# Optimization experiments

Measured on AMD Instinct MI355X. Metric: run time of the kernel, lower is better.

## Reference

```python
import jax, jax.numpy as jnp
import numpy as np

E = 1024   # embed_dim
H = 16     # num_heads
D = E // H # head_dim = 64
P = 32     # project_dim
BS = 32768


def setup_inputs() -> dict:
    key0 = jax.random.key(0)
    ks = jax.random.split(key0, 16)
    s = 0.02
    inp = {
        "query": jax.random.normal(ks[0], (BS, E), jnp.float32),
        "key": jax.random.normal(ks[1], (BS, E), jnp.float32),
        "value": jax.random.normal(ks[2], (BS, E), jnp.float32),
        "attn_bias": jax.random.normal(ks[3], (BS, H), jnp.float32),
        # q/k/v embedding linears: [E, H*D]
        "Wq": jax.random.normal(ks[4], (E, H * D), jnp.float32) * s,
        "bq": jnp.zeros((H * D,), jnp.float32),
        "Wk": jax.random.normal(ks[5], (E, H * D), jnp.float32) * s,
        "bk": jnp.zeros((H * D,), jnp.float32),
        "Wv": jax.random.normal(ks[6], (E, H * D), jnp.float32) * s,
        "bv": jnp.zeros((H * D,), jnp.float32),
        # key/value low-rank projection linears: [E, H*P]
        "We": jax.random.normal(ks[7], (E, H * P), jnp.float32) * s,
        "be": jnp.zeros((H * P,), jnp.float32),
        "Wf": jax.random.normal(ks[8], (E, H * P), jnp.float32) * s,
        "bf": jnp.zeros((H * P,), jnp.float32),
        # feature_expand: [H, H*P]
        "Wfe": jax.random.normal(ks[9], (H, H * P), jnp.float32) * s,
        "bfe": jnp.zeros((H * P,), jnp.float32),
        # out_linear: [H*D, E]
        "Wo": jax.random.normal(ks[10], (H * D, E), jnp.float32) * s,
        "bo": jnp.zeros((E,), jnp.float32),
    }
    return inp


def reference(query, key, value, attn_bias,
              Wq, bq, Wk, bk, Wv, bv,
              We, be, Wf, bf, Wfe, bfe, Wo, bo):
    bs = query.shape[0]
    scale = 1.0 / np.sqrt(D).astype(np.float32)

    q = (query @ Wq + bq).reshape(bs, H, D)   # [bs, H, D]
    k = (key @ Wk + bk).reshape(bs, H, D)     # [bs, H, D]
    v = (value @ Wv + bv).reshape(bs, H, D)   # [bs, H, D]
    e = (key @ We + be).reshape(bs, H, P)     # [bs, H, P]
    f = (value @ Wf + bf).reshape(bs, H, P)   # [bs, H, P]

    # With tgt_len=src_len=1: q @ (e @ k)^T == (q.k) * e  (outer-product collapse)
    qk = jnp.einsum('bhd,bhd->bh', q, k)                     # [bs, H]
    bias = (attn_bias @ Wfe + bfe).reshape(bs, H, P)          # [bs, H, P]
    attn = scale * qk[..., None] * e + bias                   # [bs, H, P]
    attn = jax.nn.softmax(attn, axis=-1)                      # dropout p=0 (eval)

    # attn @ (f @ v) == (attn.f) * v
    af = jnp.einsum('bhp,bhp->bh', attn, f)                   # [bs, H]
    out = (af[..., None] * v).reshape(bs, H * D) @ Wo + bo    # [bs, E]
    return out
```

## Files before the change

### kernel.cpp

```cpp
#include <hip/hip_runtime.h>
#include <hip/hip_bf16.h>
#include <stdint.h>

#define BS_N 32768
#define E_DIM 1024

typedef __bf16 bf16x8 __attribute__((ext_vector_type(8)));
typedef float f32x4 __attribute__((ext_vector_type(4)));

__device__ __forceinline__ float asf(uint32_t u){ union{uint32_t u;float f;}x; x.u=u; return x.f; }
__device__ __forceinline__ uint32_t asu(float f){ union{float f;uint32_t u;}x; x.f=f; return x.u; }
__device__ __forceinline__ float blo(uint32_t u){ return asf(u<<16); }
__device__ __forceinline__ float bhi(uint32_t u){ return asf(u & 0xffff0000u); }
__device__ __forceinline__ uint16_t f2b(float f){
  uint32_t u = asu(f);
  u = u + 0x7fffu + ((u>>16)&1u);
  return (uint16_t)(u>>16);
}
__device__ __forceinline__ uint32_t pack2(float lo, float hi){
  return (uint32_t)f2b(lo) | ((uint32_t)f2b(hi)<<16);
}

#define GLD16(g, l) __builtin_amdgcn_global_load_lds( \
    (__attribute__((address_space(1))) const void*)(g), \
    (__attribute__((address_space(3))) void*)(l), 16, 0, 0)

#define BAR() __builtin_amdgcn_s_barrier()
#define LGKM0() do{ asm volatile("s_waitcnt lgkmcnt(0)" ::: "memory"); __builtin_amdgcn_sched_barrier(0); }while(0)
#define VMC4() do{ asm volatile("s_waitcnt vmcnt(4)" ::: "memory"); __builtin_amdgcn_sched_barrier(0); }while(0)
#define VMC0() do{ asm volatile("s_waitcnt vmcnt(0)" ::: "memory"); __builtin_amdgcn_sched_barrier(0); }while(0)

__global__ __launch_bounds__(256) void cast_bf16(const float4* __restrict__ in,
                                                 uint2* __restrict__ out, int n4){
  int i = blockIdx.x*256 + threadIdx.x;
  int stride = gridDim.x*256;
  for (; i < n4; i += stride){
    float4 v = in[i];
    uint2 o; o.x = pack2(v.x, v.y); o.y = pack2(v.z, v.w);
    out[i] = o;
  }
}

__global__ __launch_bounds__(256) void transpose_cast(const float* __restrict__ W,
                                                      uint16_t* __restrict__ WT,
                                                      int R, int C){
  __shared__ float tile[32][33];
  int c0 = blockIdx.x*32, r0 = blockIdx.y*32;
  int tx = threadIdx.x, ty = threadIdx.y;
  #pragma unroll
  for (int i=0;i<32;i+=8) tile[ty+i][tx] = W[(size_t)(r0+ty+i)*C + c0+tx];
  __syncthreads();
  #pragma unroll
  for (int i=0;i<32;i+=8) WT[(size_t)(c0+ty+i)*R + r0+tx] = f2b(tile[tx][ty+i]);
}

__global__ __launch_bounds__(256) void prep_ab(const float* __restrict__ ab,
                                               uint16_t* __restrict__ abp){
  int i = blockIdx.x*256 + threadIdx.x;
  int b = i >> 5, j = i & 31;
  abp[i] = f2b(j < 16 ? ab[b*16 + j] : 0.f);
}

__global__ __launch_bounds__(256) void prep_wfe(const float* __restrict__ Wfe,
                                                uint16_t* __restrict__ WfeTp){
  int i = blockIdx.x*256 + threadIdx.x;
  int n = i >> 5, j = i & 31;
  float v = (j < 16) ? Wfe[j*512 + n] : 0.f;
  WfeTp[n*32 + j] = f2b(v);
}

__global__ __launch_bounds__(256) void cat2(const float* __restrict__ a, int na,
                                            const float* __restrict__ b, int nb,
                                            float* __restrict__ o){
  int i = blockIdx.x*256 + threadIdx.x;
  if (i < na) o[i] = a[i];
  else if (i < na + nb) o[i] = b[i - na];
}

template<int BF16OUT>
__global__ __launch_bounds__(512, 2) void gemm256(const uint16_t* __restrict__ A,
                                                  const uint16_t* __restrict__ BT,
                                                  const float* __restrict__ bias,
                                                  void* __restrict__ Cp,
                                                  int N, int K){
  __shared__ alignas(16) uint16_t As_[2][16384];
  __shared__ alignas(16) uint16_t Bs_[2][16384];

  const int tid  = threadIdx.x;
  const int lane = tid & 63;
  const int w    = tid >> 6;
  const int wm   = w >> 2;
  const int wn   = w & 3;
  const int r    = lane & 15;
  const int kc   = lane >> 4;

  int bid = (int)blockIdx.x;
  int nwg = (int)gridDim.x;
  int cpx = nwg >> 3;
  int swz = (bid & 7)*cpx + (bid >> 3);
  const int rowTile = swz & 127;
  const int colTile = swz >> 7;
  const int row0 = rowTile << 8;
  const int col0 = colTile << 8;

  f32x4 acc[8][4];
  #pragma unroll
  for (int i=0;i<8;i++)
    #pragma unroll
    for (int j=0;j<4;j++){ f32x4 z = {0.f,0.f,0.f,0.f}; acc[i][j] = z; }

  const int NT = K >> 6;
  const size_t K2 = (size_t)K * 2;

  const int sr  = tid >> 3;
  const int scS = ((tid & 7) << 4) ^ ((sr & 7) << 4);
  const char* gA = (const char*)(A  + (size_t)row0 * K) + (size_t)sr*K2 + scS;
  const char* gB = (const char*)(BT + (size_t)col0 * K) + (size_t)sr*K2 + scS;
  char* ldsA = (char*)&As_[0][0];
  char* ldsB = (char*)&Bs_[0][0];

  #define STAGE_A(b, hh, u) do{ \
    const char* s_ = gA + (size_t)(hh)*(K2<<7) + ((size_t)(u)<<7); \
    char* d_ = ldsA + ((b)<<15) + ((hh)<<14) + (tid<<4); \
    GLD16(s_, d_); GLD16(s_ + (K2<<6), d_ + 8192); }while(0)
  #define STAGE_B(b, hh, u) do{ \
    const char* s_ = gB + (size_t)(hh)*(K2<<7) + ((size_t)(u)<<7); \
    char* d_ = ldsB + ((b)<<15) + ((hh)<<14) + (tid<<4); \
    GLD16(s_, d_); GLD16(s_ + (K2<<6), d_ + 8192); }while(0)

  const int rdKey = (kc << 4) ^ ((r & 7) << 4);
  const char* aR = ldsA + ((wm*128 + r) * 128);
  const char* bR = ldsB + ((wn*64  + r) * 128);

  bf16x8 afr[4][2], bf0[2][2], bf1[2][2];

  #define READ_A(QM) do{ \
    _Pragma("unroll") for (int fm=0; fm<4; ++fm) \
    _Pragma("unroll") for (int ks=0; ks<2; ++ks) \
      afr[fm][ks] = *(const bf16x8*)(aB + (QM)*8192 + fm*2048 + (rdKey ^ (ks<<6))); }while(0)
  #define READ_B(DST, QN) do{ \
    _Pragma("unroll") for (int fn=0; fn<2; ++fn) \
    _Pragma("unroll") for (int ks=0; ks<2; ++ks) \
      DST[fn][ks] = *(const bf16x8*)(bB + (QN)*4096 + fn*2048 + (rdKey ^ (ks<<6))); }while(0)
  #define MFMA16(QM, QN, BF) do{ \
    __builtin_amdgcn_s_setprio(1); \
    _Pragma("unroll") for (int ks=0; ks<2; ++ks) \
    _Pragma("unroll") for (int fm=0; fm<4; ++fm) \
    _Pragma("unroll") for (int fn=0; fn<2; ++fn) \
      acc[(QM)*4+fm][(QN)*2+fn] = __builtin_amdgcn_mfma_f32_16x16x32_bf16( \
        afr[fm][ks], BF[fn][ks], acc[(QM)*4+fm][(QN)*2+fn], 0, 0, 0); \
    __builtin_amdgcn_s_setprio(0); }while(0)

  STAGE_B(0,0,0); STAGE_B(0,1,0); STAGE_A(0,0,0); STAGE_A(0,1,0);
  if (NT > 1){ STAGE_B(1,0,1); STAGE_B(1,1,1); VMC4(); }
  else       { VMC0(); }
  BAR();

  for (int t = 0; t < NT; ++t){
    const int buf = t & 1;
    const char* aB = aR + (buf << 15);
    const char* bB = bR + (buf << 15);
    READ_A(0); READ_B(bf0, 0);
    if (t+1 < NT) STAGE_A(buf^1, 0, t+1);
    BAR(); LGKM0();
    MFMA16(0,0,bf0);
    BAR();
    READ_B(bf1, 1);
    if (t+1 < NT) STAGE_A(buf^1, 1, t+1);
    BAR(); LGKM0();
    MFMA16(0,1,bf1);
    BAR();
    READ_A(1);
    if (t+2 < NT) STAGE_B(buf, 0, t+2);
    BAR(); LGKM0();
    MFMA16(1,0,bf0);
    BAR();
    if (t+2 < NT) STAGE_B(buf, 1, t+2);
    BAR(); LGKM0();
    MFMA16(1,1,bf1);
    if (t+2 < NT) { VMC4(); } else { VMC0(); }
    BAR();
  }

  const int crow = row0 + wm*128 + ((lane>>4)<<2);
  const int ccol = col0 + wn*64 + (lane & 15);
  #pragma unroll
  for (int i=0;i<8;i++){
    #pragma unroll
    for (int n=0;n<4;n++){
      int col = ccol + n*16;
      float bv = bias[col];
      #pragma unroll
      for (int j=0;j<4;j++){
        float val = acc[i][n][j] + bv;
        int row = crow + i*16 + j;
        if (BF16OUT) ((uint16_t*)Cp)[(size_t)row*N + col] = f2b(val);
        else         ((float*)Cp)   [(size_t)row*N + col] = val;
      }
    }
  }
  #undef STAGE_A
  #undef STAGE_B
  #undef READ_A
  #undef READ_B
  #undef MFMA16
}

template<int BF16OUT>
__global__ __launch_bounds__(256) void gemm_bt(const uint16_t* __restrict__ A,
                                               const uint16_t* __restrict__ BT,
                                               const float* __restrict__ bias,
                                               void* __restrict__ Cp,
                                               int N, int K){
  __shared__ alignas(16) uint16_t As[128*32];
  __shared__ alignas(16) uint16_t Bs[128*32];
  const int tid  = threadIdx.x;
  const int lane = tid & 63;
  const int w    = tid >> 6;
  const int wr   = w >> 1, wc = w & 1;

  int bid = (int)blockIdx.x;
  int nwg = (int)gridDim.x;
  int cpx = nwg >> 3;
  int swz = (bid & 7)*cpx + (bid >> 3);
  int rowTile = swz & 255;
  int colTile = swz >> 8;
  const size_t row0 = (size_t)rowTile << 7;
  const int col0 = colTile << 7;

  f32x4 acc[4][4];
  #pragma unroll
  for (int m=0;m<4;m++)
    #pragma unroll
    for (int n=0;n<4;n++){ f32x4 z = {0.f,0.f,0.f,0.f}; acc[m][n] = z; }

  const int c0 = tid, c1 = tid + 256;
  const int ar0 = c0 >> 2, ao0 = (c0 & 3) << 4;
  const int ar1 = c1 >> 2, ao1 = (c1 & 3) << 4;
  const size_t K2 = (size_t)K * 2;
  const char* Ab = (const char*)(A  + row0 * (size_t)K);
  const char* Bb = (const char*)(BT + (size_t)col0 * (size_t)K);
  const char* gA0 = Ab + (size_t)ar0*K2 + ao0;
  const char* gA1 = Ab + (size_t)ar1*K2 + ao1;
  const char* gB0 = Bb + (size_t)ar0*K2 + ao0;
  const char* gB1 = Bb + (size_t)ar1*K2 + ao1;
  char* lA0 = (char*)As + c0*16;
  char* lA1 = (char*)As + c1*16;
  char* lB0 = (char*)Bs + c0*16;
  char* lB1 = (char*)Bs + c1*16;

  const int r = lane & 15, kc = lane >> 4;
  const char* aRd = (const char*)As + ((wr<<6) + r)*64 + (kc<<4);
  const char* bRd = (const char*)Bs + ((wc<<6) + r)*64 + (kc<<4);

  for (int kt = 0; kt < K; kt += 32){
    GLD16(gA0 + kt*2, lA0);
    GLD16(gA1 + kt*2, lA1);
    GLD16(gB0 + kt*2, lB0);
    GLD16(gB1 + kt*2, lB1);
    __syncthreads();
    bf16x8 a[4], b[4];
    #pragma unroll
    for (int m=0;m<4;m++) a[m] = *(const bf16x8*)(aRd + m*1024);
    #pragma unroll
    for (int n=0;n<4;n++) b[n] = *(const bf16x8*)(bRd + n*1024);
    #pragma unroll
    for (int m=0;m<4;m++)
      #pragma unroll
      for (int n=0;n<4;n++)
        acc[m][n] = __builtin_amdgcn_mfma_f32_16x16x32_bf16(a[m], b[n], acc[m][n], 0, 0, 0);
    __syncthreads();
  }

  const int crow = (int)row0 + (wr<<6) + ((lane>>4)<<2);
  const int ccol = col0 + (wc<<6) + (lane & 15);
  #pragma unroll
  for (int n=0;n<4;n++){
    int col = ccol + n*16;
    float bv = bias[col];
    #pragma unroll
    for (int m=0;m<4;m++){
      #pragma unroll
      for (int j=0;j<4;j++){
        float val = acc[m][n][j] + bv;
        if (BF16OUT) ((uint16_t*)Cp)[(size_t)(crow + m*16 + j)*N + col] = f2b(val);
        else         ((float*)Cp)   [(size_t)(crow + m*16 + j)*N + col] = val;
      }
    }
  }
}

__global__ __launch_bounds__(256) void middle(const uint16_t* __restrict__ qo,
                                              const uint16_t* __restrict__ keo,
                                              const uint16_t* __restrict__ vfo,
                                              const uint16_t* __restrict__ bb,
                                              uint16_t* __restrict__ t){
  int tid = blockIdx.x*256 + threadIdx.x;
  int b = tid >> 4, h = tid & 15;

  const uint4* qp = (const uint4*)(qo  + ((size_t)b<<10) + (h<<6));
  const uint4* kp = (const uint4*)(keo + (size_t)b*1536 + (h<<6));
  float qk = 0.f;
  #pragma unroll
  for (int i=0;i<8;i++){
    uint4 x = qp[i], y = kp[i];
    qk += blo(x.x)*blo(y.x) + bhi(x.x)*bhi(y.x);
    qk += blo(x.y)*blo(y.y) + bhi(x.y)*bhi(y.y);
    qk += blo(x.z)*blo(y.z) + bhi(x.z)*bhi(y.z);
    qk += blo(x.w)*blo(y.w) + bhi(x.w)*bhi(y.w);
  }
  qk *= 0.125f;

  const uint4* ep = (const uint4*)(keo + (size_t)b*1536 + 1024 + (h<<5));
  const uint4* bp = (const uint4*)(bb  + ((size_t)b<<9) + (h<<5));
  float s[32];
  #pragma unroll
  for (int i=0;i<4;i++){
    uint4 ev = ep[i], bv = bp[i];
    s[i*8+0] = qk*blo(ev.x) + blo(bv.x);
    s[i*8+1] = qk*bhi(ev.x) + bhi(bv.x);
    s[i*8+2] = qk*blo(ev.y) + blo(bv.y);
    s[i*8+3] = qk*bhi(ev.y) + bhi(bv.y);
    s[i*8+4] = qk*blo(ev.z) + blo(bv.z);
    s[i*8+5] = qk*bhi(ev.z) + bhi(bv.z);
    s[i*8+6] = qk*blo(ev.w) + blo(bv.w);
    s[i*8+7] = qk*bhi(ev.w) + bhi(bv.w);
  }
  float mx = s[0];
  #pragma unroll
  for (int p=1;p<32;p++) mx = fmaxf(mx, s[p]);
  float sum = 0.f;
  #pragma unroll
  for (int p=0;p<32;p++){ s[p] = __expf(s[p]-mx); sum += s[p]; }

  const uint4* fp = (const uint4*)(vfo + (size_t)b*1536 + 1024 + (h<<5));
  float af = 0.f;
  #pragma unroll
  for (int i=0;i<4;i++){
    uint4 fv = fp[i];
    af += s[i*8+0]*blo(fv.x) + s[i*8+1]*bhi(fv.x);
    af += s[i*8+2]*blo(fv.y) + s[i*8+3]*bhi(fv.y);
    af += s[i*8+4]*blo(fv.z) + s[i*8+5]*bhi(fv.z);
    af += s[i*8+6]*blo(fv.w) + s[i*8+7]*bhi(fv.w);
  }
  af /= sum;

  const uint4* vp = (const uint4*)(vfo + (size_t)b*1536 + (h<<6));
  uint4* tp = (uint4*)(t + ((size_t)b<<10) + (h<<6));
  #pragma unroll
  for (int i=0;i<8;i++){
    uint4 vv = vp[i];
    uint4 o;
    o.x = pack2(af*blo(vv.x), af*bhi(vv.x));
    o.y = pack2(af*blo(vv.y), af*bhi(vv.y));
    o.z = pack2(af*blo(vv.z), af*bhi(vv.z));
    o.w = pack2(af*blo(vv.w), af*bhi(vv.w));
    tp[i] = o;
  }
}

extern "C" void kernel_launch(void* const* d_in, const int* in_sizes, int n_in,
                              void* d_out, int out_size, void* d_ws, size_t ws_size,
                              hipStream_t stream){
  const float* query = (const float*)d_in[0];
  const float* key   = (const float*)d_in[1];
  const float* value = (const float*)d_in[2];
  const float* ab    = (const float*)d_in[3];
  const float* Wq  = (const float*)d_in[4];
  const float* bq  = (const float*)d_in[5];
  const float* Wk  = (const float*)d_in[6];
  const float* bk  = (const float*)d_in[7];
  const float* Wv  = (const float*)d_in[8];
  const float* bv  = (const float*)d_in[9];
  const float* We  = (const float*)d_in[10];
  const float* be  = (const float*)d_in[11];
  const float* Wf  = (const float*)d_in[12];
  const float* bfp = (const float*)d_in[13];
  const float* Wfe = (const float*)d_in[14];
  const float* bfe = (const float*)d_in[15];
  const float* Wo  = (const float*)d_in[16];
  const float* bo  = (const float*)d_in[17];

  char* ws = (char*)d_ws;
  const size_t MB = (size_t)1 << 20;
  uint16_t* kb    = (uint16_t*)(ws +   0*MB);
  uint16_t* vb    = (uint16_t*)(ws +  64*MB);
  uint16_t* qb    = (uint16_t*)(ws + 128*MB);
  uint16_t* qo    = (uint16_t*)(ws + 192*MB);
  uint16_t* keo   = (uint16_t*)(ws + 256*MB);
  uint16_t* vfo   = (uint16_t*)(ws + 352*MB);
  uint16_t* bb    = (uint16_t*)(ws + 448*MB);
  uint16_t* abp   = (uint16_t*)(ws + 480*MB);
  uint16_t* WqT   = (uint16_t*)(ws + 482*MB);
  uint16_t* WkeT  = (uint16_t*)(ws + 484*MB);
  uint16_t* WvfT  = (uint16_t*)(ws + 487*MB);
  uint16_t* WoT   = (uint16_t*)(ws + 490*MB);
  uint16_t* WfeTp = (uint16_t*)(ws + 492*MB);
  float*    bke   = (float*)   (ws + 493*MB);
  float*    bvf   = (float*)   (ws + 493*MB + 16384);
  uint16_t* t     = qb;

  const int n4 = (BS_N*E_DIM)/4;
  cast_bf16<<<2048,256,0,stream>>>((const float4*)query, (uint2*)qb, n4);
  cast_bf16<<<2048,256,0,stream>>>((const float4*)key,   (uint2*)kb, n4);
  cast_bf16<<<2048,256,0,stream>>>((const float4*)value, (uint2*)vb, n4);

  dim3 tb(32,8);
  transpose_cast<<<dim3(32,32),tb,0,stream>>>(Wq, WqT, 1024, 1024);
  transpose_cast<<<dim3(32,32),tb,0,stream>>>(Wk, WkeT, 1024, 1024);
  transpose_cast<<<dim3(16,32),tb,0,stream>>>(We, WkeT + (size_t)1024*1024, 1024, 512);
  transpose_cast<<<dim3(32,32),tb,0,stream>>>(Wv, WvfT, 1024, 1024);
  transpose_cast<<<dim3(16,32),tb,0,stream>>>(Wf, WvfT + (size_t)1024*1024, 1024, 512);
  transpose_cast<<<dim3(32,32),tb,0,stream>>>(Wo, WoT, 1024, 1024);
  prep_ab<<<4096,256,0,stream>>>(ab, abp);
  prep_wfe<<<64,256,0,stream>>>(Wfe, WfeTp);
  cat2<<<6,256,0,stream>>>(bk, 1024, be, 512, bke);
  cat2<<<6,256,0,stream>>>(bv, 1024, bfp, 512, bvf);

  gemm256<1><<<512,512,0,stream>>>(qb, WqT,  bq,  qo,  1024, 1024);
  gemm256<1><<<768,512,0,stream>>>(kb, WkeT, bke, keo, 1536, 1024);
  gemm256<1><<<768,512,0,stream>>>(vb, WvfT, bvf, vfo, 1536, 1024);

  gemm_bt<1><<<1024,256,0,stream>>>(abp, WfeTp, bfe, bb, 512, 32);

  middle<<<2048,256,0,stream>>>(qo, keo, vfo, bb, t);

  gemm256<0><<<512,512,0,stream>>>(t, WoT, bo, d_out, 1024, 1024);
}
```

Measured before the change: 972.0 us.

## Merge input casts and QKV GEMMs into grouped launches, restage GEMM prefetch

The three fp32-to-bf16 cast kernels become one kernel over all three tensors. The three projection GEMMs become a single grouped launch of 2048 workgroups that picks its operands by column tile. Inside the GEMM body, A and B tiles are now both prefetched two iterations ahead, which deepens the vmcnt wait to 8. Epilogue stores become nontemporal. These changes aim to cut launch overhead and tail effects and to hide more global latency, at the cost of more in-flight loads and possible cache effects from the nontemporal output.

Result: slower. 1.010 ms (+3.9%).

```diff
diff --git a/kernel.cpp b/kernel.cpp
--- a/kernel.cpp
+++ b/kernel.cpp
@@ -27,17 +27,26 @@
 
 #define BAR() __builtin_amdgcn_s_barrier()
 #define LGKM0() do{ asm volatile("s_waitcnt lgkmcnt(0)" ::: "memory"); __builtin_amdgcn_sched_barrier(0); }while(0)
-#define VMC4() do{ asm volatile("s_waitcnt vmcnt(4)" ::: "memory"); __builtin_amdgcn_sched_barrier(0); }while(0)
+#define VMC8() do{ asm volatile("s_waitcnt vmcnt(8)" ::: "memory"); __builtin_amdgcn_sched_barrier(0); }while(0)
 #define VMC0() do{ asm volatile("s_waitcnt vmcnt(0)" ::: "memory"); __builtin_amdgcn_sched_barrier(0); }while(0)
 
-__global__ __launch_bounds__(256) void cast_bf16(const float4* __restrict__ in,
-                                                 uint2* __restrict__ out, int n4){
+__global__ __launch_bounds__(256) void cast3(const float4* __restrict__ q,
+                                             const float4* __restrict__ k,
+                                             const float4* __restrict__ v,
+                                             uint2* __restrict__ oq,
+                                             uint2* __restrict__ ok,
+                                             uint2* __restrict__ ov){
+  const int n4 = (BS_N*E_DIM)/4;
   int i = blockIdx.x*256 + threadIdx.x;
   int stride = gridDim.x*256;
-  for (; i < n4; i += stride){
-    float4 v = in[i];
-    uint2 o; o.x = pack2(v.x, v.y); o.y = pack2(v.z, v.w);
-    out[i] = o;
+  for (; i < 3*n4; i += stride){
+    int seg = i >> 23;
+    int j = i & (n4 - 1);
+    const float4* in = seg==0 ? q : (seg==1 ? k : v);
+    uint2* out = seg==0 ? oq : (seg==1 ? ok : ov);
+    float4 w = in[j];
+    uint2 o; o.x = pack2(w.x, w.y); o.y = pack2(w.z, w.w);
+    out[j] = o;
   }
 }
 
@@ -78,14 +87,12 @@
 }
 
 template<int BF16OUT>
-__global__ __launch_bounds__(512, 2) void gemm256(const uint16_t* __restrict__ A,
-                                                  const uint16_t* __restrict__ BT,
-                                                  const float* __restrict__ bias,
-                                                  void* __restrict__ Cp,
-                                                  int N, int K){
-  __shared__ alignas(16) uint16_t As_[2][16384];
-  __shared__ alignas(16) uint16_t Bs_[2][16384];
-
+__device__ __forceinline__ void g256_body(const uint16_t* __restrict__ A,
+                                          const uint16_t* __restrict__ BT,
+                                          const float* __restrict__ bias,
+                                          void* __restrict__ Cp,
+                                          int N, int K, int row0, int col0,
+                                          char* ldsA, char* ldsB){
   const int tid  = threadIdx.x;
   const int lane = tid & 63;
   const int w    = tid >> 6;
@@ -94,15 +101,6 @@
   const int r    = lane & 15;
   const int kc   = lane >> 4;
 
-  int bid = (int)blockIdx.x;
-  int nwg = (int)gridDim.x;
-  int cpx = nwg >> 3;
-  int swz = (bid & 7)*cpx + (bid >> 3);
-  const int rowTile = swz & 127;
-  const int colTile = swz >> 7;
-  const int row0 = rowTile << 8;
-  const int col0 = colTile << 8;
-
   f32x4 acc[8][4];
   #pragma unroll
   for (int i=0;i<8;i++)
@@ -116,8 +114,6 @@
   const int scS = ((tid & 7) << 4) ^ ((sr & 7) << 4);
   const char* gA = (const char*)(A  + (size_t)row0 * K) + (size_t)sr*K2 + scS;
   const char* gB = (const char*)(BT + (size_t)col0 * K) + (size_t)sr*K2 + scS;
-  char* ldsA = (char*)&As_[0][0];
-  char* ldsB = (char*)&Bs_[0][0];
 
   #define STAGE_A(b, hh, u) do{ \
     const char* s_ = gA + (size_t)(hh)*(K2<<7) + ((size_t)(u)<<7); \
@@ -151,8 +147,8 @@
         afr[fm][ks], BF[fn][ks], acc[(QM)*4+fm][(QN)*2+fn], 0, 0, 0); \
     __builtin_amdgcn_s_setprio(0); }while(0)
 
-  STAGE_B(0,0,0); STAGE_B(0,1,0); STAGE_A(0,0,0); STAGE_A(0,1,0);
-  if (NT > 1){ STAGE_B(1,0,1); STAGE_B(1,1,1); VMC4(); }
+  STAGE_A(0,0,0); STAGE_B(0,0,0); STAGE_B(0,1,0); STAGE_A(0,1,0);
+  if (NT > 1){ STAGE_A(1,0,1); STAGE_B(1,0,1); STAGE_B(1,1,1); STAGE_A(1,1,1); VMC8(); }
   else       { VMC0(); }
   BAR();
 
@@ -161,24 +157,22 @@
     const char* aB = aR + (buf << 15);
     const char* bB = bR + (buf << 15);
     READ_A(0); READ_B(bf0, 0);
-    if (t+1 < NT) STAGE_A(buf^1, 0, t+1);
     BAR(); LGKM0();
     MFMA16(0,0,bf0);
     BAR();
     READ_B(bf1, 1);
-    if (t+1 < NT) STAGE_A(buf^1, 1, t+1);
     BAR(); LGKM0();
     MFMA16(0,1,bf1);
     BAR();
     READ_A(1);
-    if (t+2 < NT) STAGE_B(buf, 0, t+2);
+    if (t+2 < NT){ STAGE_B(buf, 0, t+2); STAGE_B(buf, 1, t+2); }
     BAR(); LGKM0();
     MFMA16(1,0,bf0);
     BAR();
-    if (t+2 < NT) STAGE_B(buf, 1, t+2);
+    if (t+2 < NT){ STAGE_A(buf, 0, t+2); STAGE_A(buf, 1, t+2); }
     BAR(); LGKM0();
     MFMA16(1,1,bf1);
-    if (t+2 < NT) { VMC4(); } else { VMC0(); }
+    if (t+2 < NT) { VMC8(); } else { VMC0(); }
     BAR();
   }
 
@@ -194,8 +188,8 @@
       for (int j=0;j<4;j++){
         float val = acc[i][n][j] + bv;
         int row = crow + i*16 + j;
-        if (BF16OUT) ((uint16_t*)Cp)[(size_t)row*N + col] = f2b(val);
-        else         ((float*)Cp)   [(size_t)row*N + col] = val;
+        if (BF16OUT) __builtin_nontemporal_store(f2b(val), ((uint16_t*)Cp) + (size_t)row*N + col);
+        else         __builtin_nontemporal_store(val,      ((float*)Cp)    + (size_t)row*N + col);
       }
     }
   }
@@ -204,6 +198,47 @@
   #undef READ_A
   #undef READ_B
   #undef MFMA16
+}
+
+template<int BF16OUT>
+__global__ __launch_bounds__(512, 2) void gemm256s(const uint16_t* __restrict__ A,
+                                                   const uint16_t* __restrict__ BT,
+                                                   const float* __restrict__ bias,
+                                                   void* __restrict__ Cp,
+                                                   int N, int K){
+  __shared__ alignas(16) uint16_t As_[2][16384];
+  __shared__ alignas(16) uint16_t Bs_[2][16384];
+  int bid = (int)blockIdx.x;
+  int nwg = (int)gridDim.x;
+  int cpx = nwg >> 3;
+  int swz = (bid & 7)*cpx + (bid >> 3);
+  const int rowTile = swz & 127;
+  const int colTile = swz >> 7;
+  g256_body<BF16OUT>(A, BT, bias, Cp, N, K, rowTile<<8, colTile<<8,
+                     (char*)&As_[0][0], (char*)&Bs_[0][0]);
+}
+
+__global__ __launch_bounds__(512, 2) void gemm256g(
+    const uint16_t* __restrict__ A0, const uint16_t* __restrict__ A1, const uint16_t* __restrict__ A2,
+    const uint16_t* __restrict__ B0, const uint16_t* __restrict__ B1, const uint16_t* __restrict__ B2,
+    const float* __restrict__ f0, const float* __restrict__ f1, const float* __restrict__ f2,
+    uint16_t* __restrict__ C0, uint16_t* __restrict__ C1, uint16_t* __restrict__ C2,
+    int n0, int n1, int n2, int ct1, int ct2, int K){
+  __shared__ alignas(16) uint16_t As_[2][16384];
+  __shared__ alignas(16) uint16_t Bs_[2][16384];
+  int bid = (int)blockIdx.x;
+  int nwg = (int)gridDim.x;
+  int cpx = nwg >> 3;
+  int swz = (bid & 7)*cpx + (bid >> 3);
+  const int rowTile = swz & 127;
+  const int colTile = swz >> 7;
+
+  const uint16_t* A; const uint16_t* BT; const float* bias; uint16_t* C; int N; int ctl;
+  if (colTile < ct1)      { A=A0; BT=B0; bias=f0; C=C0; N=n0; ctl=colTile; }
+  else if (colTile < ct2) { A=A1; BT=B1; bias=f1; C=C1; N=n1; ctl=colTile-ct1; }
+  else                    { A=A2; BT=B2; bias=f2; C=C2; N=n2; ctl=colTile-ct2; }
+  g256_body<1>(A, BT, bias, C, N, K, rowTile<<8, ctl<<8,
+               (char*)&As_[0][0], (char*)&Bs_[0][0]);
 }
 
 template<int BF16OUT>
@@ -400,10 +435,8 @@
   float*    bvf   = (float*)   (ws + 493*MB + 16384);
   uint16_t* t     = qb;
 
-  const int n4 = (BS_N*E_DIM)/4;
-  cast_bf16<<<2048,256,0,stream>>>((const float4*)query, (uint2*)qb, n4);
-  cast_bf16<<<2048,256,0,stream>>>((const float4*)key,   (uint2*)kb, n4);
-  cast_bf16<<<2048,256,0,stream>>>((const float4*)value, (uint2*)vb, n4);
+  cast3<<<3072,256,0,stream>>>((const float4*)query, (const float4*)key, (const float4*)value,
+                               (uint2*)qb, (uint2*)kb, (uint2*)vb);
 
   dim3 tb(32,8);
   transpose_cast<<<dim3(32,32),tb,0,stream>>>(Wq, WqT, 1024, 1024);
@@ -417,13 +450,15 @@
   cat2<<<6,256,0,stream>>>(bk, 1024, be, 512, bke);
   cat2<<<6,256,0,stream>>>(bv, 1024, bfp, 512, bvf);
 
-  gemm256<1><<<512,512,0,stream>>>(qb, WqT,  bq,  qo,  1024, 1024);
-  gemm256<1><<<768,512,0,stream>>>(kb, WkeT, bke, keo, 1536, 1024);
-  gemm256<1><<<768,512,0,stream>>>(vb, WvfT, bvf, vfo, 1536, 1024);
+  gemm256g<<<2048,512,0,stream>>>(qb, kb, vb,
+                                  WqT, WkeT, WvfT,
+                                  bq, bke, bvf,
+                                  qo, keo, vfo,
+                                  1024, 1536, 1536, 4, 10, 1024);
 
   gemm_bt<1><<<1024,256,0,stream>>>(abp, WfeTp, bfe, bb, 512, 32);
 
   middle<<<2048,256,0,stream>>>(qo, keo, vfo, bb, t);
 
-  gemm256<0><<<512,512,0,stream>>>(t, WoT, bo, d_out, 1024, 1024);
-}
+  gemm256s<0><<<512,512,0,stream>>>(t, WoT, bo, d_out, 1024, 1024);
+}
```
